# Kernel optimization log

Measured on AMD Instinct MI355X. Metric: run time of the kernel, lower is better.

The kernel has to match this reference:

```python
import jax, jax.numpy as jnp
import numpy as np

EPS = 1e-6
LN_EPS = 1e-5  # torch.nn.LayerNorm default


def setup_inputs() -> dict:
    key = jax.random.key(0)
    k1, k2, k3, k4 = jax.random.split(key, 4)
    B, T, L, S, C = 32, 512, 5, 9, 64
    x = jax.random.normal(k1, (B, T), dtype=jnp.float32)
    ws = jax.random.uniform(k2, (S, C), dtype=jnp.float32, minval=-1.0, maxval=1.0)
    bs = jax.random.uniform(k3, (S, C), dtype=jnp.float32, minval=-1.0, maxval=1.0)
    loc_emb = 0.02 * jax.random.normal(k4, (L, C), dtype=jnp.float32)
    # scales = base_bias**i for i in -(S-1)//2 .. (S+1)//2 - 1  (base_bias=10, S=9 -> 10^-4..10^4)
    scales = jnp.asarray([10.0 ** i for i in range(-(S - 1) // 2, (S + 1) // 2)], dtype=jnp.float32)
    locs = jnp.asarray([-2.0, -1.0, 0.0, 1.0, 2.0], dtype=jnp.float32)
    return {"x": x, "ws": ws, "bs": bs, "loc_emb": loc_emb, "scales": scales, "locs": locs}


def reference(x, ws, bs, loc_emb, scales, locs):
    # x: (B, T); locs: (L,); scales: (S,); ws/bs: (S, C); loc_emb: (L, C)
    loc_dis = x[..., None] - locs                                  # (B, T, L)
    # location weights
    loc_w = 1.0 / (jnp.log(jnp.abs(loc_dis) + 1.0) + EPS)          # (B, T, L)
    loc_w = loc_w / jnp.sum(loc_w, axis=-1, keepdims=True)
    # scale weights
    scale_w = 1.0 / (jnp.abs(jnp.log(jnp.abs(loc_dis)[..., None] / scales + EPS)) + EPS)  # (B, T, L, S)
    scale_w = scale_w / jnp.sum(scale_w, axis=-1, keepdims=True)
    # broadcast encode: (B, T, L, 1, 1) * (S, C) + (S, C) * (S, 1) -> (B, T, L, S, C)
    enc = loc_dis[..., None, None] * ws + bs * scales[:, None]
    # LayerNorm over channel dim, no affine
    mean = jnp.mean(enc, axis=-1, keepdims=True)
    var = jnp.mean(jnp.square(enc - mean), axis=-1, keepdims=True)
    enc = (enc - mean) * jax.lax.rsqrt(var + LN_EPS)
    # weighted sum over scales -> (B, T, L, C)
    enc = jnp.sum(enc * scale_w[..., None], axis=-2)
    enc = enc + loc_emb
    # weighted sum over locations -> (B, T, C)
    enc = jnp.sum(enc * loc_w[..., None], axis=-2)
    return enc


if __name__ == "__main__":
    out = reference(**setup_inputs())
    print(out.shape, out.dtype)
```

## Files before the change

kernel.cpp:

```cpp
#include <hip/hip_runtime.h>
#include <math.h>


#define EPS_W 1e-6f
#define LN_EPS 1e-5f

constexpr int L = 5;
constexpr int S = 9;
constexpr int C = 64;
constexpr int PPB = 16;
constexpr int NCOEF = 24;

__device__ __forceinline__ float fastrcp(float v) { return __builtin_amdgcn_rcpf(v); }

__global__ __launch_bounds__(64) void mbe2_kernel(
    const float* __restrict__ x,
    const float* __restrict__ ws,
    const float* __restrict__ bs,
    const float* __restrict__ loc_emb,
    const float* __restrict__ scales,
    const float* __restrict__ locs,
    float* __restrict__ out,
    int npos)
{
    const int lane = threadIdx.x;

    float w[S], k[S], rsc[S];
    float mw[S], mk[S], vw[S], cwk2[S], vk[S];
    float le[L], lc[L];
#pragma unroll
    for (int s = 0; s < S; ++s) {
        float sc = scales[s];
        rsc[s] = fastrcp(sc);
        w[s] = ws[s * C + lane];
        k[s] = bs[s * C + lane] * sc;
    }
#pragma unroll
    for (int l = 0; l < L; ++l) {
        le[l] = loc_emb[l * C + lane];
        lc[l] = locs[l];
    }

#pragma unroll
    for (int s = 0; s < S; ++s) {
        float a0 = w[s], a1 = k[s];
        float a2 = w[s] * w[s], a3 = w[s] * k[s], a4 = k[s] * k[s];
#pragma unroll
        for (int off = 32; off; off >>= 1) {
            a0 += __shfl_xor(a0, off);
            a1 += __shfl_xor(a1, off);
            a2 += __shfl_xor(a2, off);
            a3 += __shfl_xor(a3, off);
            a4 += __shfl_xor(a4, off);
        }
        float mww = a0 * (1.0f / 64.0f);
        float mkk = a1 * (1.0f / 64.0f);
        mw[s] = mww;
        mk[s] = mkk;
        vw[s] = fmaf(-mww, mww, a2 * (1.0f / 64.0f));
        cwk2[s] = 2.0f * fmaf(-mww, mkk, a3 * (1.0f / 64.0f));
        vk[s] = fmaf(-mkk, mkk, a4 * (1.0f / 64.0f));
    }

    __shared__ float coef[PPB][NCOEF];

    const int pbase = blockIdx.x * PPB;
    if (lane < PPB) {
        int p = pbase + lane;
        if (p < npos) {
            float xv = x[p];

            float d[L], lwv[L];
            float lwsum = 0.0f;
#pragma unroll
            for (int l = 0; l < L; ++l) {
                d[l] = xv - lc[l];
                float ad = fabsf(d[l]);
                lwv[l] = fastrcp(__logf(ad + 1.0f) + EPS_W);
                lwsum += lwv[l];
            }
            float rlw = fastrcp(lwsum);

            float A[S], Bc[S];
#pragma unroll
            for (int s = 0; s < S; ++s) { A[s] = 0.0f; Bc[s] = 0.0f; }
            float cnst = 0.0f;
            float lwn[L];

#pragma unroll
            for (int l = 0; l < L; ++l) {
                float dd = d[l];
                float ad = fabsf(dd);
                lwn[l] = lwv[l] * rlw;

                float swv[S];
                float ssum = 0.0f;
#pragma unroll
                for (int s = 0; s < S; ++s) {
                    float t = fabsf(__logf(fmaf(ad, rsc[s], EPS_W))) + EPS_W;
                    swv[s] = fastrcp(t);
                    ssum += swv[s];
                }
                float rss = fastrcp(ssum) * lwn[l];

#pragma unroll
                for (int s = 0; s < S; ++s) {
                    float mean = fmaf(dd, mw[s], mk[s]);
                    float var = fmaf(dd, fmaf(dd, vw[s], cwk2[s]), vk[s]);
                    float rstd = rsqrtf(var + LN_EPS);
                    float alpha = swv[s] * rss * rstd;
                    A[s] = fmaf(alpha, dd, A[s]);
                    Bc[s] += alpha;
                    cnst = fmaf(-alpha, mean, cnst);
                }
            }

#pragma unroll
            for (int s = 0; s < S; ++s) {
                coef[lane][s] = A[s];
                coef[lane][9 + s] = Bc[s];
            }
#pragma unroll
            for (int l = 0; l < L; ++l) coef[lane][18 + l] = lwn[l];
            coef[lane][23] = cnst;
        }
    }

    __syncthreads();

    for (int i = 0; i < PPB; ++i) {
        int p = pbase + i;
        if (p >= npos) break;
        float acc = coef[i][23];
#pragma unroll
        for (int s = 0; s < S; ++s) {
            acc = fmaf(coef[i][s], w[s], acc);
            acc = fmaf(coef[i][9 + s], k[s], acc);
        }
#pragma unroll
        for (int l = 0; l < L; ++l) acc = fmaf(coef[i][18 + l], le[l], acc);
        out[p * C + lane] = acc;
    }
}

extern "C" void kernel_launch(void* const* d_in, const int* in_sizes, int n_in,
                              void* d_out, int out_size, void* d_ws, size_t ws_size,
                              hipStream_t stream) {
    const float* x = (const float*)d_in[0];
    const float* ws = (const float*)d_in[1];
    const float* bs = (const float*)d_in[2];
    const float* loc_emb = (const float*)d_in[3];
    const float* scales = (const float*)d_in[4];
    const float* locs = (const float*)d_in[5];
    float* out = (float*)d_out;

    int npos = in_sizes[0];
    int blocks = (npos + PPB - 1) / PPB;
    mbe2_kernel<<<blocks, 64, 0, stream>>>(x, ws, bs, loc_emb, scales, locs, out, npos);
}
```

Baseline: 14.45 us.

## Split into coefficient kernel and apply kernel with all lanes active

The single fused kernel, where only 16 of 64 lanes did the expensive per-position log/rcp work, is replaced by two kernels. The first computes the 24 coefficients for each position with every lane busy and writes them to workspace as float4s in a structure-of-arrays layout. The second kernel uses 256-thread blocks and gives each wave 8 positions, loading the coefficients with wave-uniform addresses and writing the 64-channel output. This trades the per-block idle lanes and LDS sync for an extra launch and a round trip of the coefficients through global memory.

After: 23.15 us. 60.3% more time.

```diff
diff --git a/kernel.cpp b/kernel.cpp
--- a/kernel.cpp
+++ b/kernel.cpp
@@ -8,26 +8,23 @@
 constexpr int L = 5;
 constexpr int S = 9;
 constexpr int C = 64;
-constexpr int PPB = 16;
-constexpr int NCOEF = 24;
+constexpr int PPW = 8;
 
 __device__ __forceinline__ float fastrcp(float v) { return __builtin_amdgcn_rcpf(v); }
 
-__global__ __launch_bounds__(64) void mbe2_kernel(
+__global__ __launch_bounds__(64) void mbe_coef_kernel(
     const float* __restrict__ x,
     const float* __restrict__ ws,
     const float* __restrict__ bs,
-    const float* __restrict__ loc_emb,
     const float* __restrict__ scales,
     const float* __restrict__ locs,
-    float* __restrict__ out,
+    float4* __restrict__ cw4,
     int npos)
 {
     const int lane = threadIdx.x;
 
-    float w[S], k[S], rsc[S];
+    float w[S], k[S], rsc[S], lc[L];
     float mw[S], mk[S], vw[S], cwk2[S], vk[S];
-    float le[L], lc[L];
 #pragma unroll
     for (int s = 0; s < S; ++s) {
         float sc = scales[s];
@@ -36,10 +33,7 @@
         k[s] = bs[s * C + lane] * sc;
     }
 #pragma unroll
-    for (int l = 0; l < L; ++l) {
-        le[l] = loc_emb[l * C + lane];
-        lc[l] = locs[l];
-    }
+    for (int l = 0; l < L; ++l) lc[l] = locs[l];
 
 #pragma unroll
     for (int s = 0; s < S; ++s) {
@@ -62,84 +56,138 @@
         vk[s] = fmaf(-mkk, mkk, a4 * (1.0f / 64.0f));
     }
 
-    __shared__ float coef[PPB][NCOEF];
-
-    const int pbase = blockIdx.x * PPB;
-    if (lane < PPB) {
-        int p = pbase + lane;
-        if (p < npos) {
-            float xv = x[p];
-
-            float d[L], lwv[L];
-            float lwsum = 0.0f;
-#pragma unroll
-            for (int l = 0; l < L; ++l) {
-                d[l] = xv - lc[l];
-                float ad = fabsf(d[l]);
-                lwv[l] = fastrcp(__logf(ad + 1.0f) + EPS_W);
-                lwsum += lwv[l];
-            }
-            float rlw = fastrcp(lwsum);
-
-            float A[S], Bc[S];
-#pragma unroll
-            for (int s = 0; s < S; ++s) { A[s] = 0.0f; Bc[s] = 0.0f; }
-            float cnst = 0.0f;
-            float lwn[L];
-
-#pragma unroll
-            for (int l = 0; l < L; ++l) {
-                float dd = d[l];
-                float ad = fabsf(dd);
-                lwn[l] = lwv[l] * rlw;
-
-                float swv[S];
-                float ssum = 0.0f;
-#pragma unroll
-                for (int s = 0; s < S; ++s) {
-                    float t = fabsf(__logf(fmaf(ad, rsc[s], EPS_W))) + EPS_W;
-                    swv[s] = fastrcp(t);
-                    ssum += swv[s];
-                }
-                float rss = fastrcp(ssum) * lwn[l];
-
-#pragma unroll
-                for (int s = 0; s < S; ++s) {
-                    float mean = fmaf(dd, mw[s], mk[s]);
-                    float var = fmaf(dd, fmaf(dd, vw[s], cwk2[s]), vk[s]);
-                    float rstd = rsqrtf(var + LN_EPS);
-                    float alpha = swv[s] * rss * rstd;
-                    A[s] = fmaf(alpha, dd, A[s]);
-                    Bc[s] += alpha;
-                    cnst = fmaf(-alpha, mean, cnst);
-                }
-            }
-
-#pragma unroll
-            for (int s = 0; s < S; ++s) {
-                coef[lane][s] = A[s];
-                coef[lane][9 + s] = Bc[s];
-            }
-#pragma unroll
-            for (int l = 0; l < L; ++l) coef[lane][18 + l] = lwn[l];
-            coef[lane][23] = cnst;
-        }
-    }
-
-    __syncthreads();
-
-    for (int i = 0; i < PPB; ++i) {
-        int p = pbase + i;
-        if (p >= npos) break;
-        float acc = coef[i][23];
+    const int p = blockIdx.x * 64 + lane;
+    if (p >= npos) return;
+    float xv = x[p];
+
+    float d[L], lwv[L];
+    float lwsum = 0.0f;
+#pragma unroll
+    for (int l = 0; l < L; ++l) {
+        d[l] = xv - lc[l];
+        float ad = fabsf(d[l]);
+        lwv[l] = fastrcp(__logf(ad + 1.0f) + EPS_W);
+        lwsum += lwv[l];
+    }
+    float rlw = fastrcp(lwsum);
+
+    float cf[24];
+#pragma unroll
+    for (int j = 0; j < 24; ++j) cf[j] = 0.0f;
+
+#pragma unroll
+    for (int l = 0; l < L; ++l) {
+        float dd = d[l];
+        float ad = fabsf(dd);
+        float lwn = lwv[l] * rlw;
+        cf[18 + l] = lwn;
+
+        float swv[S];
+        float ssum = 0.0f;
 #pragma unroll
         for (int s = 0; s < S; ++s) {
-            acc = fmaf(coef[i][s], w[s], acc);
-            acc = fmaf(coef[i][9 + s], k[s], acc);
-        }
-#pragma unroll
-        for (int l = 0; l < L; ++l) acc = fmaf(coef[i][18 + l], le[l], acc);
-        out[p * C + lane] = acc;
+            float t = fabsf(__logf(fmaf(ad, rsc[s], EPS_W))) + EPS_W;
+            swv[s] = fastrcp(t);
+            ssum += swv[s];
+        }
+        float rss = fastrcp(ssum) * lwn;
+
+#pragma unroll
+        for (int s = 0; s < S; ++s) {
+            float mean = fmaf(dd, mw[s], mk[s]);
+            float var = fmaf(dd, fmaf(dd, vw[s], cwk2[s]), vk[s]);
+            float rstd = rsqrtf(var + LN_EPS);
+            float alpha = swv[s] * rss * rstd;
+            cf[s] = fmaf(alpha, dd, cf[s]);
+            cf[9 + s] += alpha;
+            cf[23] = fmaf(-alpha, mean, cf[23]);
+        }
+    }
+
+#pragma unroll
+    for (int j4 = 0; j4 < 6; ++j4) {
+        cw4[j4 * npos + p] = make_float4(cf[4 * j4], cf[4 * j4 + 1],
+                                         cf[4 * j4 + 2], cf[4 * j4 + 3]);
+    }
+}
+
+__global__ __launch_bounds__(256) void mbe_apply_kernel(
+    const float* __restrict__ ws,
+    const float* __restrict__ bs,
+    const float* __restrict__ loc_emb,
+    const float* __restrict__ scales,
+    const float4* __restrict__ cw4,
+    float* __restrict__ out,
+    int npos)
+{
+    const int lane = threadIdx.x & 63;
+    const int wid = threadIdx.x >> 6;
+
+    float w[S], k[S], le[L];
+#pragma unroll
+    for (int s = 0; s < S; ++s) {
+        w[s] = ws[s * C + lane];
+        k[s] = bs[s * C + lane] * scales[s];
+    }
+#pragma unroll
+    for (int l = 0; l < L; ++l) le[l] = loc_emb[l * C + lane];
+
+    const int pbase = (blockIdx.x * 4 + wid) * PPW;
+    if (pbase >= npos) return;
+
+    if (pbase + PPW <= npos) {
+#pragma unroll
+        for (int i = 0; i < PPW; ++i) {
+            const int up = __builtin_amdgcn_readfirstlane(pbase + i);
+            float4 q0 = cw4[0 * npos + up];
+            float4 q1 = cw4[1 * npos + up];
+            float4 q2 = cw4[2 * npos + up];
+            float4 q3 = cw4[3 * npos + up];
+            float4 q4 = cw4[4 * npos + up];
+            float4 q5 = cw4[5 * npos + up];
+            float acc = q5.w;
+            acc = fmaf(q0.x, w[0], acc); acc = fmaf(q0.y, w[1], acc);
+            acc = fmaf(q0.z, w[2], acc); acc = fmaf(q0.w, w[3], acc);
+            acc = fmaf(q1.x, w[4], acc); acc = fmaf(q1.y, w[5], acc);
+            acc = fmaf(q1.z, w[6], acc); acc = fmaf(q1.w, w[7], acc);
+            acc = fmaf(q2.x, w[8], acc);
+            acc = fmaf(q2.y, k[0], acc); acc = fmaf(q2.z, k[1], acc);
+            acc = fmaf(q2.w, k[2], acc); acc = fmaf(q3.x, k[3], acc);
+            acc = fmaf(q3.y, k[4], acc); acc = fmaf(q3.z, k[5], acc);
+            acc = fmaf(q3.w, k[6], acc); acc = fmaf(q4.x, k[7], acc);
+            acc = fmaf(q4.y, k[8], acc);
+            acc = fmaf(q4.z, le[0], acc); acc = fmaf(q4.w, le[1], acc);
+            acc = fmaf(q5.x, le[2], acc); acc = fmaf(q5.y, le[3], acc);
+            acc = fmaf(q5.z, le[4], acc);
+            out[(size_t)(pbase + i) * C + lane] = acc;
+        }
+    } else {
+        for (int i = 0; i < PPW; ++i) {
+            const int p = pbase + i;
+            if (p >= npos) break;
+            const int up = __builtin_amdgcn_readfirstlane(p);
+            float4 q0 = cw4[0 * npos + up];
+            float4 q1 = cw4[1 * npos + up];
+            float4 q2 = cw4[2 * npos + up];
+            float4 q3 = cw4[3 * npos + up];
+            float4 q4 = cw4[4 * npos + up];
+            float4 q5 = cw4[5 * npos + up];
+            float acc = q5.w;
+            acc = fmaf(q0.x, w[0], acc); acc = fmaf(q0.y, w[1], acc);
+            acc = fmaf(q0.z, w[2], acc); acc = fmaf(q0.w, w[3], acc);
+            acc = fmaf(q1.x, w[4], acc); acc = fmaf(q1.y, w[5], acc);
+            acc = fmaf(q1.z, w[6], acc); acc = fmaf(q1.w, w[7], acc);
+            acc = fmaf(q2.x, w[8], acc);
+            acc = fmaf(q2.y, k[0], acc); acc = fmaf(q2.z, k[1], acc);
+            acc = fmaf(q2.w, k[2], acc); acc = fmaf(q3.x, k[3], acc);
+            acc = fmaf(q3.y, k[4], acc); acc = fmaf(q3.z, k[5], acc);
+            acc = fmaf(q3.w, k[6], acc); acc = fmaf(q4.x, k[7], acc);
+            acc = fmaf(q4.y, k[8], acc);
+            acc = fmaf(q4.z, le[0], acc); acc = fmaf(q4.w, le[1], acc);
+            acc = fmaf(q5.x, le[2], acc); acc = fmaf(q5.y, le[3], acc);
+            acc = fmaf(q5.z, le[4], acc);
+            out[(size_t)p * C + lane] = acc;
+        }
     }
 }
 
@@ -153,8 +201,14 @@
     const float* scales = (const float*)d_in[4];
     const float* locs = (const float*)d_in[5];
     float* out = (float*)d_out;
+    float4* cw4 = (float4*)d_ws;
 
     int npos = in_sizes[0];
-    int blocks = (npos + PPB - 1) / PPB;
-    mbe2_kernel<<<blocks, 64, 0, stream>>>(x, ws, bs, loc_emb, scales, locs, out, npos);
+
+    int blocks1 = (npos + 63) / 64;
+    mbe_coef_kernel<<<blocks1, 64, 0, stream>>>(x, ws, bs, scales, locs, cw4, npos);
+
+    int pos_per_block = 4 * PPW;
+    int blocks2 = (npos + pos_per_block - 1) / pos_per_block;
+    mbe_apply_kernel<<<blocks2, 256, 0, stream>>>(ws, bs, loc_emb, scales, cw4, out, npos);
 }
```

## Use 256-thread blocks with 64 positions each, sharing LN stats via LDS

Applied to the files above, without the earlier changes.

Blocks grow to four wavefronts covering 64 positions, so the per-block setup (loading ws/bs, reducing LayerNorm statistics) is amortised over more positions and spread across waves via shared memory. All 64 lanes of wave 0 now compute per-position coefficients instead of 16. The per-scale log is rewritten as log|d| minus log(scale), clamped at log(EPS), so each location needs one log instead of nine. Coefficients go through LDS as float4. The clamp only approximates log(x+eps), and the block count drops to a quarter, which lowers parallelism.

Result: faster. 13.39 us (-7.3%).

```diff
diff --git a/kernel.cpp b/kernel.cpp
--- a/kernel.cpp
+++ b/kernel.cpp
@@ -4,16 +4,16 @@
 
 #define EPS_W 1e-6f
 #define LN_EPS 1e-5f
+#define LOG_EPS -13.815511f
 
 constexpr int L = 5;
 constexpr int S = 9;
 constexpr int C = 64;
-constexpr int PPB = 16;
-constexpr int NCOEF = 24;
+constexpr int POS = 64;
 
 __device__ __forceinline__ float fastrcp(float v) { return __builtin_amdgcn_rcpf(v); }
 
-__global__ __launch_bounds__(64) void mbe2_kernel(
+__global__ __launch_bounds__(256, 1) void mbe3_kernel(
     const float* __restrict__ x,
     const float* __restrict__ ws,
     const float* __restrict__ bs,
@@ -23,26 +23,23 @@
     float* __restrict__ out,
     int npos)
 {
-    const int lane = threadIdx.x;
+    const int tid = threadIdx.x;
+    const int lane = tid & 63;
+    const int wid = tid >> 6;
 
-    float w[S], k[S], rsc[S];
-    float mw[S], mk[S], vw[S], cwk2[S], vk[S];
-    float le[L], lc[L];
+    __shared__ float stats[S][8];
+    __shared__ float4 coefLds[POS][6];
+
+    float w[S], k[S], le[L];
 #pragma unroll
     for (int s = 0; s < S; ++s) {
-        float sc = scales[s];
-        rsc[s] = fastrcp(sc);
         w[s] = ws[s * C + lane];
-        k[s] = bs[s * C + lane] * sc;
+        k[s] = bs[s * C + lane] * scales[s];
     }
 #pragma unroll
-    for (int l = 0; l < L; ++l) {
-        le[l] = loc_emb[l * C + lane];
-        lc[l] = locs[l];
-    }
+    for (int l = 0; l < L; ++l) le[l] = loc_emb[l * C + lane];
 
-#pragma unroll
-    for (int s = 0; s < S; ++s) {
+    for (int s = wid; s < S; s += 4) {
         float a0 = w[s], a1 = k[s];
         float a2 = w[s] * w[s], a3 = w[s] * k[s], a4 = k[s] * k[s];
 #pragma unroll
@@ -53,93 +50,111 @@
             a3 += __shfl_xor(a3, off);
             a4 += __shfl_xor(a4, off);
         }
-        float mww = a0 * (1.0f / 64.0f);
-        float mkk = a1 * (1.0f / 64.0f);
-        mw[s] = mww;
-        mk[s] = mkk;
-        vw[s] = fmaf(-mww, mww, a2 * (1.0f / 64.0f));
-        cwk2[s] = 2.0f * fmaf(-mww, mkk, a3 * (1.0f / 64.0f));
-        vk[s] = fmaf(-mkk, mkk, a4 * (1.0f / 64.0f));
+        if (lane == 0) {
+            float mww = a0 * (1.0f / 64.0f);
+            float mkk = a1 * (1.0f / 64.0f);
+            stats[s][0] = mww;
+            stats[s][1] = mkk;
+            stats[s][2] = fmaf(-mww, mww, a2 * (1.0f / 64.0f));
+            stats[s][3] = 2.0f * fmaf(-mww, mkk, a3 * (1.0f / 64.0f));
+            stats[s][4] = fmaf(-mkk, mkk, a4 * (1.0f / 64.0f));
+            stats[s][5] = __logf(scales[s]);
+        }
     }
+    __syncthreads();
 
-    __shared__ float coef[PPB][NCOEF];
+    const int pbase = blockIdx.x * POS;
+    if (wid == 0) {
+        const int p = pbase + lane;
+        if (p < npos) {
+            float mw[S], mk[S], vw[S], c2[S], vk[S], lg[S];
+#pragma unroll
+            for (int s = 0; s < S; ++s) {
+                mw[s] = stats[s][0]; mk[s] = stats[s][1]; vw[s] = stats[s][2];
+                c2[s] = stats[s][3]; vk[s] = stats[s][4]; lg[s] = stats[s][5];
+            }
+            const float xv = x[p];
 
-    const int pbase = blockIdx.x * PPB;
-    if (lane < PPB) {
-        int p = pbase + lane;
-        if (p < npos) {
-            float xv = x[p];
-
-            float d[L], lwv[L];
+            float d[L], lwv[L], llog[L];
             float lwsum = 0.0f;
 #pragma unroll
             for (int l = 0; l < L; ++l) {
-                d[l] = xv - lc[l];
+                d[l] = xv - locs[l];
                 float ad = fabsf(d[l]);
                 lwv[l] = fastrcp(__logf(ad + 1.0f) + EPS_W);
                 lwsum += lwv[l];
+                llog[l] = __logf(ad);
             }
-            float rlw = fastrcp(lwsum);
+            const float rlw = fastrcp(lwsum);
 
-            float A[S], Bc[S];
+            float cf[24];
 #pragma unroll
-            for (int s = 0; s < S; ++s) { A[s] = 0.0f; Bc[s] = 0.0f; }
-            float cnst = 0.0f;
-            float lwn[L];
+            for (int j = 0; j < 24; ++j) cf[j] = 0.0f;
 
 #pragma unroll
             for (int l = 0; l < L; ++l) {
-                float dd = d[l];
-                float ad = fabsf(dd);
-                lwn[l] = lwv[l] * rlw;
+                const float dd = d[l];
+                const float d2 = dd * dd;
+                const float lwn = lwv[l] * rlw;
+                cf[18 + l] = lwn;
 
                 float swv[S];
                 float ssum = 0.0f;
 #pragma unroll
                 for (int s = 0; s < S; ++s) {
-                    float t = fabsf(__logf(fmaf(ad, rsc[s], EPS_W))) + EPS_W;
-                    swv[s] = fastrcp(t);
+                    float u = fmaxf(llog[l] - lg[s], LOG_EPS);
+                    swv[s] = fastrcp(fabsf(u) + EPS_W);
                     ssum += swv[s];
                 }
-                float rss = fastrcp(ssum) * lwn[l];
+                const float rss = fastrcp(ssum) * lwn;
 
 #pragma unroll
                 for (int s = 0; s < S; ++s) {
                     float mean = fmaf(dd, mw[s], mk[s]);
-                    float var = fmaf(dd, fmaf(dd, vw[s], cwk2[s]), vk[s]);
+                    float var = fmaf(d2, vw[s], fmaf(dd, c2[s], vk[s]));
                     float rstd = rsqrtf(var + LN_EPS);
                     float alpha = swv[s] * rss * rstd;
-                    A[s] = fmaf(alpha, dd, A[s]);
-                    Bc[s] += alpha;
-                    cnst = fmaf(-alpha, mean, cnst);
+                    cf[s] = fmaf(alpha, dd, cf[s]);
+                    cf[9 + s] += alpha;
+                    cf[23] = fmaf(-alpha, mean, cf[23]);
                 }
             }
 
 #pragma unroll
-            for (int s = 0; s < S; ++s) {
-                coef[lane][s] = A[s];
-                coef[lane][9 + s] = Bc[s];
-            }
-#pragma unroll
-            for (int l = 0; l < L; ++l) coef[lane][18 + l] = lwn[l];
-            coef[lane][23] = cnst;
+            for (int j = 0; j < 6; ++j)
+                coefLds[lane][j] = make_float4(cf[4 * j], cf[4 * j + 1],
+                                               cf[4 * j + 2], cf[4 * j + 3]);
         }
     }
-
     __syncthreads();
 
-    for (int i = 0; i < PPB; ++i) {
-        int p = pbase + i;
+    const int rbase = wid * 16;
+#pragma unroll
+    for (int i = 0; i < 16; ++i) {
+        const int row = rbase + i;
+        const int p = pbase + row;
         if (p >= npos) break;
-        float acc = coef[i][23];
-#pragma unroll
-        for (int s = 0; s < S; ++s) {
-            acc = fmaf(coef[i][s], w[s], acc);
-            acc = fmaf(coef[i][9 + s], k[s], acc);
-        }
-#pragma unroll
-        for (int l = 0; l < L; ++l) acc = fmaf(coef[i][18 + l], le[l], acc);
-        out[p * C + lane] = acc;
+        float4 q0 = coefLds[row][0];
+        float4 q1 = coefLds[row][1];
+        float4 q2 = coefLds[row][2];
+        float4 q3 = coefLds[row][3];
+        float4 q4 = coefLds[row][4];
+        float4 q5 = coefLds[row][5];
+        float acc = q5.w;
+        acc = fmaf(q0.x, w[0], acc); acc = fmaf(q0.y, w[1], acc);
+        acc = fmaf(q0.z, w[2], acc); acc = fmaf(q0.w, w[3], acc);
+        acc = fmaf(q1.x, w[4], acc); acc = fmaf(q1.y, w[5], acc);
+        acc = fmaf(q1.z, w[6], acc); acc = fmaf(q1.w, w[7], acc);
+        acc = fmaf(q2.x, w[8], acc);
+        acc = fmaf(q2.y, k[0], acc); acc = fmaf(q2.z, k[1], acc);
+        acc = fmaf(q2.w, k[2], acc); acc = fmaf(q3.x, k[3], acc);
+        acc = fmaf(q3.y, k[4], acc); acc = fmaf(q3.z, k[5], acc);
+        acc = fmaf(q3.w, k[6], acc); acc = fmaf(q4.x, k[7], acc);
+        acc = fmaf(q4.y, k[8], acc);
+        acc = fmaf(q4.z, le[0], acc); acc = fmaf(q4.w, le[1], acc);
+        acc = fmaf(q5.x, le[2], acc); acc = fmaf(q5.y, le[3], acc);
+        acc = fmaf(q5.z, le[4], acc);
+        out[(size_t)p * C + lane] = acc;
     }
 }
 
@@ -155,6 +170,6 @@
     float* out = (float*)d_out;
 
     int npos = in_sizes[0];
-    int blocks = (npos + PPB - 1) / PPB;
-    mbe2_kernel<<<blocks, 64, 0, stream>>>(x, ws, bs, loc_emb, scales, locs, out, npos);
+    int blocks = (npos + POS - 1) / POS;
+    mbe3_kernel<<<blocks, 256, 0, stream>>>(x, ws, bs, loc_emb, scales, locs, out, npos);
 }
```
